# Kernel optimization log

Hardware: AMD Instinct MI355X
Metric: run time of the kernel (lower is better)

The kernel has to match this reference:

```python
import jax, jax.numpy as jnp
import numpy as np

B, N, FIN, FOUT, N_TASKS = 32, 1024, 1024, 1024, 16

def setup_inputs() -> dict:
    key = jax.random.key(0)
    k1, k2, k3 = jax.random.split(key, 3)
    x = jax.random.normal(k1, (B, N, FIN), dtype=jnp.float32)
    task_id = jax.random.randint(k2, (B,), 0, N_TASKS, dtype=jnp.int64)
    # Embedding table: one flattened [fout*fin] weight matrix per task
    # (kaiming-style scale for 'relu' init, matching get_rnd_weight intent)
    scale = np.sqrt(2.0 / FIN).astype(np.float32)
    W = jax.random.normal(k3, (N_TASKS, FOUT * FIN), dtype=jnp.float32) * scale
    return {"x": x, "task_id": task_id, "W": W}

def reference(x, task_id, W):
    # gather per-sample weight: [B, fout, fin]
    w = W[task_id].reshape(-1, FOUT, FIN)
    # axis == 2: contract over feature dim d=fin
    out = jnp.einsum('bnd,bcd->bnc', x, w)  # [B, N, fout]
    return (out, task_id)
```

## Files before the change

### kernel.cpp

```cpp
#include <hip/hip_runtime.h>

typedef _Float16 f16;
typedef _Float16 f16x8 __attribute__((ext_vector_type(8)));
typedef __fp16   h16x2 __attribute__((ext_vector_type(2)));
typedef float    f32x4 __attribute__((ext_vector_type(4)));

constexpr int NB = 32, NN = 1024, KK = 1024, MO = 1024;
constexpr int BM = 128, BN = 128, BK = 32;
constexpr int LDA = 40;
constexpr int NSTEP = KK / BK;

__global__ __launch_bounds__(256, 2)
void cond_linear_kernel(const float* __restrict__ x,
                        const int* __restrict__ task_id,
                        const float* __restrict__ W,
                        float* __restrict__ out) {
    __shared__ __align__(16) f16 As[2][BM * LDA];
    __shared__ __align__(16) f16 Bs[2][BN * LDA];

    const int bid   = blockIdx.x;
    const int batch = bid >> 6;
    const int tile  = bid & 63;
    const int tm = tile & 7;
    const int tn = tile >> 3;

    const int tid  = threadIdx.x;
    const int task = task_id[batch];

    const float* xb = x + (size_t)batch * NN * KK + (size_t)(tm * BM) * KK;
    const float* wb = W + (size_t)task * MO * KK + (size_t)(tn * BN) * KK;

    const int c0 = tid, c1 = tid + 256;
    const int r0 = c0 >> 2, ko0 = (c0 & 3) * 8;
    const int r1 = c1 >> 2, ko1 = (c1 & 3) * 8;

    const float* pa0 = xb + r0 * KK + ko0;
    const float* pa1 = xb + r1 * KK + ko1;
    const float* pb0 = wb + r0 * KK + ko0;
    const float* pb1 = wb + r1 * KK + ko1;

    f32x4 ra0[4], rb0[4], ra1[4], rb1[4];

    auto load0 = [&](int k0) {
        ra0[0] = *(const f32x4*)(pa0 + k0); ra0[1] = *(const f32x4*)(pa0 + k0 + 4);
        ra0[2] = *(const f32x4*)(pa1 + k0); ra0[3] = *(const f32x4*)(pa1 + k0 + 4);
        rb0[0] = *(const f32x4*)(pb0 + k0); rb0[1] = *(const f32x4*)(pb0 + k0 + 4);
        rb0[2] = *(const f32x4*)(pb1 + k0); rb0[3] = *(const f32x4*)(pb1 + k0 + 4);
    };
    auto load1 = [&](int k0) {
        ra1[0] = *(const f32x4*)(pa0 + k0); ra1[1] = *(const f32x4*)(pa0 + k0 + 4);
        ra1[2] = *(const f32x4*)(pa1 + k0); ra1[3] = *(const f32x4*)(pa1 + k0 + 4);
        rb1[0] = *(const f32x4*)(pb0 + k0); rb1[1] = *(const f32x4*)(pb0 + k0 + 4);
        rb1[2] = *(const f32x4*)(pb1 + k0); rb1[3] = *(const f32x4*)(pb1 + k0 + 4);
    };

    auto cvt8 = [](const f32x4& lo, const f32x4& hi) -> f16x8 {
        union { h16x2 h[4]; f16x8 v; } u;
        u.h[0] = __builtin_amdgcn_cvt_pkrtz(lo[0], lo[1]);
        u.h[1] = __builtin_amdgcn_cvt_pkrtz(lo[2], lo[3]);
        u.h[2] = __builtin_amdgcn_cvt_pkrtz(hi[0], hi[1]);
        u.h[3] = __builtin_amdgcn_cvt_pkrtz(hi[2], hi[3]);
        return u.v;
    };

    auto store0 = [&](int buf) {
        *(f16x8*)&As[buf][r0 * LDA + ko0] = cvt8(ra0[0], ra0[1]);
        *(f16x8*)&As[buf][r1 * LDA + ko1] = cvt8(ra0[2], ra0[3]);
        *(f16x8*)&Bs[buf][r0 * LDA + ko0] = cvt8(rb0[0], rb0[1]);
        *(f16x8*)&Bs[buf][r1 * LDA + ko1] = cvt8(rb0[2], rb0[3]);
    };
    auto store1 = [&](int buf) {
        *(f16x8*)&As[buf][r0 * LDA + ko0] = cvt8(ra1[0], ra1[1]);
        *(f16x8*)&As[buf][r1 * LDA + ko1] = cvt8(ra1[2], ra1[3]);
        *(f16x8*)&Bs[buf][r0 * LDA + ko0] = cvt8(rb1[0], rb1[1]);
        *(f16x8*)&Bs[buf][r1 * LDA + ko1] = cvt8(rb1[2], rb1[3]);
    };

    auto lds_barrier = [] {
        asm volatile("s_waitcnt lgkmcnt(0)" ::: "memory");
        __builtin_amdgcn_s_barrier();
    };

    const int lane = tid & 63;
    const int wave = tid >> 6;
    const int wr   = (wave >> 1) * 64;
    const int wc   = (wave & 1) * 64;
    const int lm   = lane & 15;
    const int lq   = lane >> 4;

    f32x4 acc[4][4] = {};

    const int fa_off = (wr + lm) * LDA + lq * 8;
    const int fb_off = (wc + lm) * LDA + lq * 8;

    auto compute = [&](int buf) {
        f16x8 af[4], bf[4];
        #pragma unroll
        for (int i = 0; i < 4; ++i) af[i] = *(const f16x8*)&As[buf][fa_off + i * 16 * LDA];
        #pragma unroll
        for (int j = 0; j < 4; ++j) bf[j] = *(const f16x8*)&Bs[buf][fb_off + j * 16 * LDA];
        #pragma unroll
        for (int i = 0; i < 4; ++i)
            #pragma unroll
            for (int j = 0; j < 4; ++j)
                acc[i][j] = __builtin_amdgcn_mfma_f32_16x16x32_f16(af[i], bf[j], acc[i][j], 0, 0, 0);
    };

    load0(0);
    load1(BK);
    store0(0);
    lds_barrier();

    for (int ks = 0; ks < NSTEP; ks += 2) {
        if (ks + 2 < NSTEP) load0((ks + 2) * BK);
        compute(0);
        store1(1);
        lds_barrier();
        if (ks + 3 < NSTEP) load1((ks + 3) * BK);
        compute(1);
        if (ks + 2 < NSTEP) store0(0);
        lds_barrier();
    }

    float* ob = out + (size_t)batch * NN * MO + (size_t)(tm * BM) * MO + (tn * BN);
    #pragma unroll
    for (int i = 0; i < 4; ++i) {
        #pragma unroll
        for (int j = 0; j < 4; ++j) {
            const int row0 = wr + i * 16 + lq * 4;
            const int col  = wc + j * 16 + lm;
            #pragma unroll
            for (int r = 0; r < 4; ++r)
                ob[(size_t)(row0 + r) * MO + col] = acc[i][j][r];
        }
    }

    if (tile == 0 && tid == 0)
        out[(size_t)NB * NN * MO + batch] = (float)task;
}

extern "C" void kernel_launch(void* const* d_in, const int* in_sizes, int n_in,
                              void* d_out, int out_size, void* d_ws, size_t ws_size,
                              hipStream_t stream) {
    const float* x       = (const float*)d_in[0];
    const int*   task_id = (const int*)d_in[1];
    const float* W       = (const float*)d_in[2];
    float*       out     = (float*)d_out;

    dim3 grid(NB * (NN / BM) * (MO / BN));
    dim3 block(256);
    cond_linear_kernel<<<grid, block, 0, stream>>>(x, task_id, W, out);
}
```

Before: 371.6 us.

## Double K-tile depth to 64 and simplify to single register prefetch buffer

Raises the K tile from 32 to 64 (LDS stride 72), halving the number of barrier-separated iterations. Each stage now runs two MFMA sub-steps per buffer. The two register staging sets are merged into one, so prefetch is only one tile ahead instead of two. This cuts barrier and loop overhead and frees registers, at the cost of more LDS use and less latency hiding for the global loads.

Result: slower. 392.2 us (+5.5%).

```diff
diff --git a/kernel.cpp b/kernel.cpp
--- a/kernel.cpp
+++ b/kernel.cpp
@@ -6,8 +6,8 @@
 typedef float    f32x4 __attribute__((ext_vector_type(4)));
 
 constexpr int NB = 32, NN = 1024, KK = 1024, MO = 1024;
-constexpr int BM = 128, BN = 128, BK = 32;
-constexpr int LDA = 40;
+constexpr int BM = 128, BN = 128, BK = 64;
+constexpr int LDA = 72;
 constexpr int NSTEP = KK / BK;
 
 __global__ __launch_bounds__(256, 2)
@@ -30,28 +30,22 @@
     const float* xb = x + (size_t)batch * NN * KK + (size_t)(tm * BM) * KK;
     const float* wb = W + (size_t)task * MO * KK + (size_t)(tn * BN) * KK;
 
-    const int c0 = tid, c1 = tid + 256;
-    const int r0 = c0 >> 2, ko0 = (c0 & 3) * 8;
-    const int r1 = c1 >> 2, ko1 = (c1 & 3) * 8;
+    const int r0 = tid >> 3;
+    const int ko = (tid & 7) * 8;
 
-    const float* pa0 = xb + r0 * KK + ko0;
-    const float* pa1 = xb + r1 * KK + ko1;
-    const float* pb0 = wb + r0 * KK + ko0;
-    const float* pb1 = wb + r1 * KK + ko1;
+    const float* pa = xb + (size_t)r0 * KK + ko;
+    const float* pb = wb + (size_t)r0 * KK + ko;
 
-    f32x4 ra0[4], rb0[4], ra1[4], rb1[4];
+    f32x4 ra[8], rb[8];
 
-    auto load0 = [&](int k0) {
-        ra0[0] = *(const f32x4*)(pa0 + k0); ra0[1] = *(const f32x4*)(pa0 + k0 + 4);
-        ra0[2] = *(const f32x4*)(pa1 + k0); ra0[3] = *(const f32x4*)(pa1 + k0 + 4);
-        rb0[0] = *(const f32x4*)(pb0 + k0); rb0[1] = *(const f32x4*)(pb0 + k0 + 4);
-        rb0[2] = *(const f32x4*)(pb1 + k0); rb0[3] = *(const f32x4*)(pb1 + k0 + 4);
-    };
-    auto load1 = [&](int k0) {
-        ra1[0] = *(const f32x4*)(pa0 + k0); ra1[1] = *(const f32x4*)(pa0 + k0 + 4);
-        ra1[2] = *(const f32x4*)(pa1 + k0); ra1[3] = *(const f32x4*)(pa1 + k0 + 4);
-        rb1[0] = *(const f32x4*)(pb0 + k0); rb1[1] = *(const f32x4*)(pb0 + k0 + 4);
-        rb1[2] = *(const f32x4*)(pb1 + k0); rb1[3] = *(const f32x4*)(pb1 + k0 + 4);
+    auto load = [&](int k0) {
+        #pragma unroll
+        for (int m = 0; m < 4; ++m) {
+            ra[2 * m]     = *(const f32x4*)(pa + (size_t)m * 32 * KK + k0);
+            ra[2 * m + 1] = *(const f32x4*)(pa + (size_t)m * 32 * KK + k0 + 4);
+            rb[2 * m]     = *(const f32x4*)(pb + (size_t)m * 32 * KK + k0);
+            rb[2 * m + 1] = *(const f32x4*)(pb + (size_t)m * 32 * KK + k0 + 4);
+        }
     };
 
     auto cvt8 = [](const f32x4& lo, const f32x4& hi) -> f16x8 {
@@ -63,17 +57,12 @@
         return u.v;
     };
 
-    auto store0 = [&](int buf) {
-        *(f16x8*)&As[buf][r0 * LDA + ko0] = cvt8(ra0[0], ra0[1]);
-        *(f16x8*)&As[buf][r1 * LDA + ko1] = cvt8(ra0[2], ra0[3]);
-        *(f16x8*)&Bs[buf][r0 * LDA + ko0] = cvt8(rb0[0], rb0[1]);
-        *(f16x8*)&Bs[buf][r1 * LDA + ko1] = cvt8(rb0[2], rb0[3]);
-    };
-    auto store1 = [&](int buf) {
-        *(f16x8*)&As[buf][r0 * LDA + ko0] = cvt8(ra1[0], ra1[1]);
-        *(f16x8*)&As[buf][r1 * LDA + ko1] = cvt8(ra1[2], ra1[3]);
-        *(f16x8*)&Bs[buf][r0 * LDA + ko0] = cvt8(rb1[0], rb1[1]);
-        *(f16x8*)&Bs[buf][r1 * LDA + ko1] = cvt8(rb1[2], rb1[3]);
+    auto store = [&](int buf) {
+        #pragma unroll
+        for (int m = 0; m < 4; ++m) {
+            *(f16x8*)&As[buf][(r0 + m * 32) * LDA + ko] = cvt8(ra[2 * m], ra[2 * m + 1]);
+            *(f16x8*)&Bs[buf][(r0 + m * 32) * LDA + ko] = cvt8(rb[2 * m], rb[2 * m + 1]);
+        }
     };
 
     auto lds_barrier = [] {
@@ -94,31 +83,33 @@
     const int fb_off = (wc + lm) * LDA + lq * 8;
 
     auto compute = [&](int buf) {
-        f16x8 af[4], bf[4];
         #pragma unroll
-        for (int i = 0; i < 4; ++i) af[i] = *(const f16x8*)&As[buf][fa_off + i * 16 * LDA];
-        #pragma unroll
-        for (int j = 0; j < 4; ++j) bf[j] = *(const f16x8*)&Bs[buf][fb_off + j * 16 * LDA];
-        #pragma unroll
-        for (int i = 0; i < 4; ++i)
+        for (int kh = 0; kh < 2; ++kh) {
+            f16x8 af[4], bf[4];
             #pragma unroll
-            for (int j = 0; j < 4; ++j)
-                acc[i][j] = __builtin_amdgcn_mfma_f32_16x16x32_f16(af[i], bf[j], acc[i][j], 0, 0, 0);
+            for (int i = 0; i < 4; ++i) af[i] = *(const f16x8*)&As[buf][fa_off + i * 16 * LDA + kh * 32];
+            #pragma unroll
+            for (int j = 0; j < 4; ++j) bf[j] = *(const f16x8*)&Bs[buf][fb_off + j * 16 * LDA + kh * 32];
+            #pragma unroll
+            for (int i = 0; i < 4; ++i)
+                #pragma unroll
+                for (int j = 0; j < 4; ++j)
+                    acc[i][j] = __builtin_amdgcn_mfma_f32_16x16x32_f16(af[i], bf[j], acc[i][j], 0, 0, 0);
+        }
     };
 
-    load0(0);
-    load1(BK);
-    store0(0);
+    load(0);
+    store(0);
     lds_barrier();
 
     for (int ks = 0; ks < NSTEP; ks += 2) {
-        if (ks + 2 < NSTEP) load0((ks + 2) * BK);
+        load(1 * BK + ks * BK);
         compute(0);
-        store1(1);
+        store(1);
         lds_barrier();
-        if (ks + 3 < NSTEP) load1((ks + 3) * BK);
+        if (ks + 2 < NSTEP) load((ks + 2) * BK);
         compute(1);
-        if (ks + 2 < NSTEP) store0(0);
+        if (ks + 2 < NSTEP) store(0);
         lds_barrier();
     }
 
```
